# Optimization experiments

Measured on AMD Instinct MI355X. Metric: run time of the kernel, lower is better.

The kernel has to match this reference:

```python
import jax, jax.numpy as jnp
import numpy as np


def setup_inputs() -> dict:
    key = jax.random.key(0)
    kq, kk, kv, km = jax.random.split(key, 4)
    B, H, S, D = 2, 16, 2048, 64
    Q = jax.random.normal(kq, (B, H, S, D), dtype=jnp.float32)
    K = jax.random.normal(kk, (B, H, S, D), dtype=jnp.float32)
    V = jax.random.normal(kv, (B, H, S, D), dtype=jnp.float32)
    mask = jax.random.randint(km, (B, 1, S, S), 0, 2).astype(jnp.bool_)
    return {"Q": Q, "K": K, "V": V, "mask": mask}


def reference(Q, K, V, mask):
    # scores: [B, H, Sq, Sk]
    scores = jnp.einsum("bhqd,bhkd->bhqk", Q, K)
    neg = jnp.finfo(scores.dtype).min
    # Faithful to original: mask fill happens BEFORE the sqrt(d) scaling.
    scores = jnp.where(mask, neg, scores)
    inv_sqrt_d = 1.0 / jnp.sqrt(jnp.asarray(Q.shape[-1], dtype=scores.dtype))
    attn = jax.nn.softmax(scores * inv_sqrt_d, axis=-1)
    return jnp.einsum("bhqk,bhkd->bhqd", attn, V)
```

## Files before the change

kernel.cpp:

```cpp
#include <hip/hip_runtime.h>
#include <stdint.h>


#define SQ 2048
#define DH 64

using bf16x8  = __attribute__((ext_vector_type(8)))  __bf16;
using f32x4   = __attribute__((ext_vector_type(4)))  float;
using ushort8 = __attribute__((ext_vector_type(8)))  unsigned short;
using ushort4v= __attribute__((ext_vector_type(4)))  unsigned short;

static __device__ __forceinline__ unsigned short f2bf(float f) {
    union { float f; uint32_t u; } c; c.f = f;
    return (unsigned short)((c.u + 0x8000u) >> 16);
}

static __device__ __forceinline__ int swz(int row, int col) {
    return row * 64 + ((((col >> 3) ^ (row & 7))) << 3) + (col & 7);
}

static __device__ __forceinline__ f32x4 mfma16(bf16x8 a, bf16x8 b, f32x4 c) {
    return __builtin_amdgcn_mfma_f32_16x16x32_bf16(a, b, c, 0, 0, 0);
}

__global__ void pack_mask_kernel(const int* __restrict__ mask,
                                 unsigned long long* __restrict__ words, int nwords) {
    int gid = blockIdx.x * blockDim.x + threadIdx.x;
    int w = gid >> 6;
    int l = gid & 63;
    if (w < nwords) {
        int mv = mask[(size_t)w * 64 + l];
        unsigned long long b = __ballot(mv != 0);
        if (l == 0) words[w] = b;
    }
}

__global__ __launch_bounds__(256, 4)
void attn_kernel(const float* __restrict__ Q, const float* __restrict__ K,
                 const float* __restrict__ V,
                 const unsigned long long* __restrict__ Mw,
                 float* __restrict__ out) {
    __shared__ __align__(16) unsigned short Ks[64 * 64];
    __shared__ __align__(16) unsigned short Vt[64 * 64];
    __shared__ __align__(16) unsigned short Ps[4 * 16 * 64];

    const int tid  = threadIdx.x;
    const int w    = tid >> 6;
    const int l    = tid & 63;
    const int quad = l >> 4;
    const int c16  = l & 15;
    const int bx = blockIdx.x;
    const int hh = bx & 15;
    const int b  = (bx >> 4) & 1;
    const int qt = bx >> 5;

    const size_t bh = (size_t)b * 16 + hh;
    const float* Qp = Q + bh * SQ * DH;
    const float* Kp = K + bh * SQ * DH;
    const float* Vp = V + bh * SQ * DH;
    const int qw = qt * 64 + 16 * w;
    const unsigned long long* Mq = Mw + ((size_t)b * SQ + qw + quad * 4) * (SQ / 64);

    bf16x8 qf[2];
    {
        const float* qr = Qp + (size_t)(qw + c16) * DH;
        #pragma unroll
        for (int c = 0; c < 2; ++c) {
            int d0 = 32 * c + 8 * quad;
            float4 a  = *(const float4*)(qr + d0);
            float4 b4 = *(const float4*)(qr + d0 + 4);
            ushort8 t;
            t[0]=f2bf(a.x);  t[1]=f2bf(a.y);  t[2]=f2bf(a.z);  t[3]=f2bf(a.w);
            t[4]=f2bf(b4.x); t[5]=f2bf(b4.y); t[6]=f2bf(b4.z); t[7]=f2bf(b4.w);
            qf[c] = __builtin_bit_cast(bf16x8, t);
        }
    }

    f32x4 o[4];
    float lsum[4];
    #pragma unroll
    for (int i = 0; i < 4; ++i) { o[i] = (f32x4)(0.f); lsum[i] = 0.f; }

    unsigned short* Pw = Ps + w * (16 * 64);
    const int xg = (c16 & 7);

    for (int t = 0; t < 32; ++t) {
        const int kt0 = t * 64;

        unsigned long long mws[4];
        #pragma unroll
        for (int r = 0; r < 4; ++r) mws[r] = Mq[(size_t)r * (SQ / 64) + t];

        __syncthreads();

        #pragma unroll
        for (int i = 0; i < 4; ++i) {
            int idx = tid + 256 * i;
            int key = idx >> 4;
            int d0  = (idx & 15) << 2;
            float4 kv = *(const float4*)(Kp + (size_t)(kt0 + key) * DH + d0);
            ushort4v tt;
            tt[0]=f2bf(kv.x); tt[1]=f2bf(kv.y); tt[2]=f2bf(kv.z); tt[3]=f2bf(kv.w);
            *(ushort4v*)&Ks[swz(key, d0)] = tt;
        }
        #pragma unroll
        for (int p = 0; p < 4; ++p) {
            int k0l = 16 * w + 4 * p;
            const float* vb = Vp + (size_t)(kt0 + k0l) * DH + l;
            float x0 = vb[0], x1 = vb[DH], x2 = vb[2*DH], x3 = vb[3*DH];
            ushort4v tt;
            tt[0]=f2bf(x0); tt[1]=f2bf(x1); tt[2]=f2bf(x2); tt[3]=f2bf(x3);
            *(ushort4v*)&Vt[swz(l, k0l)] = tt;
        }
        __syncthreads();

        f32x4 s[4];
        #pragma unroll
        for (int i = 0; i < 4; ++i) s[i] = (f32x4)(0.f);
        #pragma unroll
        for (int c = 0; c < 2; ++c) {
            int g = ((4 * c + quad) ^ xg) << 3;
            #pragma unroll
            for (int nb = 0; nb < 4; ++nb) {
                bf16x8 kb = __builtin_bit_cast(bf16x8,
                    *(const ushort8*)&Ks[(c16 + 16 * nb) * 64 + g]);
                s[nb] = mfma16(qf[c], kb, s[nb]);
            }
        }

        #pragma unroll
        for (int r = 0; r < 4; ++r) {
            int row = quad * 4 + r;
            unsigned lo = (unsigned)mws[r];
            unsigned hi = (unsigned)(mws[r] >> 32);
            #pragma unroll
            for (int nb = 0; nb < 4; ++nb) {
                float e = __builtin_amdgcn_exp2f(fmaf(s[nb][r], 0.18033688f, -5.7707802f));
                unsigned bits = (nb & 2) ? hi : lo;
                unsigned bit  = 1u << (c16 + 16 * (nb & 1));
                float pv = (bits & bit) ? 0.0f : e;
                lsum[r] += pv;
                Pw[swz(row, c16 + 16 * nb)] = f2bf(pv);
            }
        }

        bf16x8 pa[2];
        #pragma unroll
        for (int c = 0; c < 2; ++c)
            pa[c] = __builtin_bit_cast(bf16x8,
                *(const ushort8*)&Pw[c16 * 64 + (((4 * c + quad) ^ xg) << 3)]);
        #pragma unroll
        for (int c = 0; c < 2; ++c) {
            int g = ((4 * c + quad) ^ xg) << 3;
            #pragma unroll
            for (int db = 0; db < 4; ++db) {
                bf16x8 vb = __builtin_bit_cast(bf16x8,
                    *(const ushort8*)&Vt[(c16 + 16 * db) * 64 + g]);
                o[db] = mfma16(pa[c], vb, o[db]);
            }
        }
    }

    #pragma unroll
    for (int r = 0; r < 4; ++r) {
        float v = lsum[r];
        v += __shfl_xor(v, 1, 64);
        v += __shfl_xor(v, 2, 64);
        v += __shfl_xor(v, 4, 64);
        v += __shfl_xor(v, 8, 64);
        float rinv = 1.0f / v;
        float* op = out + (bh * SQ + (size_t)(qw + quad * 4 + r)) * DH + c16;
        #pragma unroll
        for (int db = 0; db < 4; ++db) op[16 * db] = o[db][r] * rinv;
    }
}

extern "C" void kernel_launch(void* const* d_in, const int* in_sizes, int n_in,
                              void* d_out, int out_size, void* d_ws, size_t ws_size,
                              hipStream_t stream) {
    const float* Q    = (const float*)d_in[0];
    const float* K    = (const float*)d_in[1];
    const float* V    = (const float*)d_in[2];
    const int*   mask = (const int*)d_in[3];
    float* out = (float*)d_out;
    unsigned long long* mwords = (unsigned long long*)d_ws;

    const int nwords = 2 * SQ * (SQ / 64);
    pack_mask_kernel<<<dim3((nwords * 64) / 256), dim3(256), 0, stream>>>(mask, mwords, nwords);
    attn_kernel<<<dim3(1024), dim3(256), 0, stream>>>(Q, K, V, mwords, out);
}
```

Baseline: 190.6 us.

## Split key dimension across two blocks with atomic accumulation and normalize pass

```diff
diff --git a/kernel.cpp b/kernel.cpp
--- a/kernel.cpp
+++ b/kernel.cpp
@@ -39,7 +39,7 @@
 void attn_kernel(const float* __restrict__ Q, const float* __restrict__ K,
                  const float* __restrict__ V,
                  const unsigned long long* __restrict__ Mw,
-                 float* __restrict__ out) {
+                 float* __restrict__ outNum, float* __restrict__ sums) {
     __shared__ __align__(16) unsigned short Ks[64 * 64];
     __shared__ __align__(16) unsigned short Vt[64 * 64];
     __shared__ __align__(16) unsigned short Ps[4 * 16 * 64];
@@ -52,14 +52,16 @@
     const int bx = blockIdx.x;
     const int hh = bx & 15;
     const int b  = (bx >> 4) & 1;
-    const int qt = bx >> 5;
+    const int qt = (bx >> 5) & 31;
+    const int ks = bx >> 10;
 
     const size_t bh = (size_t)b * 16 + hh;
     const float* Qp = Q + bh * SQ * DH;
     const float* Kp = K + bh * SQ * DH;
     const float* Vp = V + bh * SQ * DH;
     const int qw = qt * 64 + 16 * w;
-    const unsigned long long* Mq = Mw + ((size_t)b * SQ + qw + quad * 4) * (SQ / 64);
+    const unsigned long long* Mq = Mw + ((size_t)b * SQ + qw + quad * 4) * (SQ / 64)
+                                      + ks * 16;
 
     bf16x8 qf[2];
     {
@@ -84,8 +86,8 @@
     unsigned short* Pw = Ps + w * (16 * 64);
     const int xg = (c16 & 7);
 
-    for (int t = 0; t < 32; ++t) {
-        const int kt0 = t * 64;
+    for (int t = 0; t < 16; ++t) {
+        const int kt0 = ks * 1024 + t * 64;
 
         unsigned long long mws[4];
         #pragma unroll
@@ -168,11 +170,22 @@
         v += __shfl_xor(v, 2, 64);
         v += __shfl_xor(v, 4, 64);
         v += __shfl_xor(v, 8, 64);
-        float rinv = 1.0f / v;
-        float* op = out + (bh * SQ + (size_t)(qw + quad * 4 + r)) * DH + c16;
-        #pragma unroll
-        for (int db = 0; db < 4; ++db) op[16 * db] = o[db][r] * rinv;
-    }
+        size_t rowg = bh * SQ + (size_t)(qw + quad * 4 + r);
+        float* op = outNum + rowg * DH + c16;
+        #pragma unroll
+        for (int db = 0; db < 4; ++db) atomicAdd(&op[16 * db], o[db][r]);
+        if (c16 == 0) atomicAdd(&sums[rowg], v);
+    }
+}
+
+__global__ __launch_bounds__(256)
+void normalize_kernel(float* __restrict__ out, const float* __restrict__ sums) {
+    int gid = blockIdx.x * 256 + threadIdx.x;
+    float rinv = 1.0f / sums[gid >> 4];
+    float4* o4 = (float4*)out;
+    float4 v = o4[gid];
+    v.x *= rinv; v.y *= rinv; v.z *= rinv; v.w *= rinv;
+    o4[gid] = v;
 }
 
 extern "C" void kernel_launch(void* const* d_in, const int* in_sizes, int n_in,
@@ -184,8 +197,12 @@
     const int*   mask = (const int*)d_in[3];
     float* out = (float*)d_out;
     unsigned long long* mwords = (unsigned long long*)d_ws;
+    float* sums = (float*)((char*)d_ws + (1 << 20));
 
     const int nwords = 2 * SQ * (SQ / 64);
+    hipMemsetAsync(d_out, 0, (size_t)out_size * sizeof(float), stream);
+    hipMemsetAsync(sums, 0, 32 * SQ * sizeof(float), stream);
     pack_mask_kernel<<<dim3((nwords * 64) / 256), dim3(256), 0, stream>>>(mask, mwords, nwords);
-    attn_kernel<<<dim3(1024), dim3(256), 0, stream>>>(Q, K, V, mwords, out);
-}
+    attn_kernel<<<dim3(2048), dim3(256), 0, stream>>>(Q, K, V, mwords, out, sums);
+    normalize_kernel<<<dim3(out_size / (4 * 256)), dim3(256), 0, stream>>>(out, sums);
+}
```

After: 213.0 us. +11.8%, slower.

## Pre-pack K to bf16 and V transposed, read MFMA operands from global

Applied to the files above, without the earlier changes.

```diff
diff --git a/kernel.cpp b/kernel.cpp
--- a/kernel.cpp
+++ b/kernel.cpp
@@ -35,35 +35,77 @@
     }
 }
 
-__global__ __launch_bounds__(256, 4)
-void attn_kernel(const float* __restrict__ Q, const float* __restrict__ K,
-                 const float* __restrict__ V,
+__global__ __launch_bounds__(256)
+void pack_kb_kernel(const float* __restrict__ K, unsigned short* __restrict__ Kb) {
+    size_t gid = (size_t)blockIdx.x * 256 + threadIdx.x;
+    const float* src = K + gid * 8;
+    float4 a = *(const float4*)src;
+    float4 b = *(const float4*)(src + 4);
+    ushort8 t;
+    t[0]=f2bf(a.x); t[1]=f2bf(a.y); t[2]=f2bf(a.z); t[3]=f2bf(a.w);
+    t[4]=f2bf(b.x); t[5]=f2bf(b.y); t[6]=f2bf(b.z); t[7]=f2bf(b.w);
+    *(ushort8*)(Kb + gid * 8) = t;
+}
+
+__global__ __launch_bounds__(256)
+void pack_vt_kernel(const float* __restrict__ V, unsigned short* __restrict__ Vt) {
+    __shared__ unsigned short L[64 * 68];
+    const int bx = blockIdx.x;
+    const int bh = bx >> 5;
+    const int kt = bx & 31;
+    const float* Vp = V + ((size_t)bh * SQ + kt * 64) * DH;
+    const int t = threadIdx.x;
+    #pragma unroll
+    for (int i = 0; i < 4; ++i) {
+        int idx = t + 256 * i;
+        int key = idx >> 4;
+        int d0  = (idx & 15) << 2;
+        float4 v = *(const float4*)&Vp[(size_t)key * DH + d0];
+        ushort4v u;
+        u[0]=f2bf(v.x); u[1]=f2bf(v.y); u[2]=f2bf(v.z); u[3]=f2bf(v.w);
+        *(ushort4v*)&L[key * 68 + d0] = u;
+    }
+    __syncthreads();
+    #pragma unroll
+    for (int i = 0; i < 2; ++i) {
+        int p  = t + 256 * i;
+        int d  = p >> 3;
+        int k8 = p & 7;
+        ushort8 o;
+        #pragma unroll
+        for (int j = 0; j < 8; ++j) o[j] = L[(8 * k8 + j) * 68 + d];
+        *(ushort8*)&Vt[((size_t)bh * DH + d) * SQ + kt * 64 + k8 * 8] = o;
+    }
+}
+
+__global__ __launch_bounds__(64, 2)
+void attn_kernel(const float* __restrict__ Q,
+                 const unsigned short* __restrict__ Kb,
+                 const unsigned short* __restrict__ Vt,
                  const unsigned long long* __restrict__ Mw,
                  float* __restrict__ out) {
-    __shared__ __align__(16) unsigned short Ks[64 * 64];
-    __shared__ __align__(16) unsigned short Vt[64 * 64];
-    __shared__ __align__(16) unsigned short Ps[4 * 16 * 64];
-
-    const int tid  = threadIdx.x;
-    const int w    = tid >> 6;
-    const int l    = tid & 63;
+    __shared__ __align__(16) unsigned short Ps[32 * 64];
+
+    const int l    = threadIdx.x;
     const int quad = l >> 4;
     const int c16  = l & 15;
+    const int xg   = c16 & 7;
     const int bx = blockIdx.x;
     const int hh = bx & 15;
     const int b  = (bx >> 4) & 1;
     const int qt = bx >> 5;
+    const int qw = qt * 32;
 
     const size_t bh = (size_t)b * 16 + hh;
     const float* Qp = Q + bh * SQ * DH;
-    const float* Kp = K + bh * SQ * DH;
-    const float* Vp = V + bh * SQ * DH;
-    const int qw = qt * 64 + 16 * w;
-    const unsigned long long* Mq = Mw + ((size_t)b * SQ + qw + quad * 4) * (SQ / 64);
-
-    bf16x8 qf[2];
-    {
-        const float* qr = Qp + (size_t)(qw + c16) * DH;
+    const unsigned short* Kbp = Kb + bh * SQ * DH;
+    const unsigned short* Vtp = Vt + bh * DH * SQ;
+    const unsigned long long* Mq = Mw + ((size_t)b * SQ + qw + 4 * quad) * (SQ / 64);
+
+    bf16x8 qf[2][2];
+    #pragma unroll
+    for (int f = 0; f < 2; ++f) {
+        const float* qr = Qp + (size_t)(qw + 16 * f + c16) * DH;
         #pragma unroll
         for (int c = 0; c < 2; ++c) {
             int d0 = 32 * c + 8 * quad;
@@ -72,106 +114,92 @@
             ushort8 t;
             t[0]=f2bf(a.x);  t[1]=f2bf(a.y);  t[2]=f2bf(a.z);  t[3]=f2bf(a.w);
             t[4]=f2bf(b4.x); t[5]=f2bf(b4.y); t[6]=f2bf(b4.z); t[7]=f2bf(b4.w);
-            qf[c] = __builtin_bit_cast(bf16x8, t);
-        }
-    }
-
-    f32x4 o[4];
-    float lsum[4];
-    #pragma unroll
-    for (int i = 0; i < 4; ++i) { o[i] = (f32x4)(0.f); lsum[i] = 0.f; }
-
-    unsigned short* Pw = Ps + w * (16 * 64);
-    const int xg = (c16 & 7);
+            qf[f][c] = __builtin_bit_cast(bf16x8, t);
+        }
+    }
+
+    f32x4 o[2][4];
+    float lsum[2][4];
+    #pragma unroll
+    for (int f = 0; f < 2; ++f)
+        #pragma unroll
+        for (int i = 0; i < 4; ++i) { o[f][i] = (f32x4)(0.f); lsum[f][i] = 0.f; }
 
     for (int t = 0; t < 32; ++t) {
-        const int kt0 = t * 64;
-
-        unsigned long long mws[4];
-        #pragma unroll
-        for (int r = 0; r < 4; ++r) mws[r] = Mq[(size_t)r * (SQ / 64) + t];
-
-        __syncthreads();
-
-        #pragma unroll
-        for (int i = 0; i < 4; ++i) {
-            int idx = tid + 256 * i;
-            int key = idx >> 4;
-            int d0  = (idx & 15) << 2;
-            float4 kv = *(const float4*)(Kp + (size_t)(kt0 + key) * DH + d0);
-            ushort4v tt;
-            tt[0]=f2bf(kv.x); tt[1]=f2bf(kv.y); tt[2]=f2bf(kv.z); tt[3]=f2bf(kv.w);
-            *(ushort4v*)&Ks[swz(key, d0)] = tt;
-        }
-        #pragma unroll
-        for (int p = 0; p < 4; ++p) {
-            int k0l = 16 * w + 4 * p;
-            const float* vb = Vp + (size_t)(kt0 + k0l) * DH + l;
-            float x0 = vb[0], x1 = vb[DH], x2 = vb[2*DH], x3 = vb[3*DH];
-            ushort4v tt;
-            tt[0]=f2bf(x0); tt[1]=f2bf(x1); tt[2]=f2bf(x2); tt[3]=f2bf(x3);
-            *(ushort4v*)&Vt[swz(l, k0l)] = tt;
-        }
-        __syncthreads();
-
-        f32x4 s[4];
-        #pragma unroll
-        for (int i = 0; i < 4; ++i) s[i] = (f32x4)(0.f);
+        f32x4 s[2][4];
+        #pragma unroll
+        for (int f = 0; f < 2; ++f)
+            #pragma unroll
+            for (int i = 0; i < 4; ++i) s[f][i] = (f32x4)(0.f);
+        const unsigned short* Kt = Kbp + (size_t)t * (64 * DH);
+        #pragma unroll
+        for (int c = 0; c < 2; ++c) {
+            #pragma unroll
+            for (int nb = 0; nb < 4; ++nb) {
+                bf16x8 kb = __builtin_bit_cast(bf16x8,
+                    *(const ushort8*)&Kt[(16 * nb + c16) * DH + 32 * c + 8 * quad]);
+                s[0][nb] = mfma16(qf[0][c], kb, s[0][nb]);
+                s[1][nb] = mfma16(qf[1][c], kb, s[1][nb]);
+            }
+        }
+
+        unsigned long long mws[2][4];
+        #pragma unroll
+        for (int f = 0; f < 2; ++f)
+            #pragma unroll
+            for (int r = 0; r < 4; ++r)
+                mws[f][r] = Mq[(size_t)(16 * f + r) * (SQ / 64) + t];
+
+        #pragma unroll
+        for (int f = 0; f < 2; ++f) {
+            #pragma unroll
+            for (int r = 0; r < 4; ++r) {
+                int row = 16 * f + 4 * quad + r;
+                unsigned lo = (unsigned)mws[f][r];
+                unsigned hi = (unsigned)(mws[f][r] >> 32);
+                #pragma unroll
+                for (int nb = 0; nb < 4; ++nb) {
+                    float e = __builtin_amdgcn_exp2f(
+                        fmaf(s[f][nb][r], 0.18033688f, -5.7707802f));
+                    unsigned bits = (nb & 2) ? hi : lo;
+                    unsigned bit  = 1u << (c16 + 16 * (nb & 1));
+                    float pv = (bits & bit) ? 0.0f : e;
+                    lsum[f][r] += pv;
+                    Ps[swz(row, c16 + 16 * nb)] = f2bf(pv);
+                }
+            }
+        }
+
         #pragma unroll
         for (int c = 0; c < 2; ++c) {
             int g = ((4 * c + quad) ^ xg) << 3;
-            #pragma unroll
-            for (int nb = 0; nb < 4; ++nb) {
-                bf16x8 kb = __builtin_bit_cast(bf16x8,
-                    *(const ushort8*)&Ks[(c16 + 16 * nb) * 64 + g]);
-                s[nb] = mfma16(qf[c], kb, s[nb]);
-            }
-        }
-
-        #pragma unroll
-        for (int r = 0; r < 4; ++r) {
-            int row = quad * 4 + r;
-            unsigned lo = (unsigned)mws[r];
-            unsigned hi = (unsigned)(mws[r] >> 32);
-            #pragma unroll
-            for (int nb = 0; nb < 4; ++nb) {
-                float e = __builtin_amdgcn_exp2f(fmaf(s[nb][r], 0.18033688f, -5.7707802f));
-                unsigned bits = (nb & 2) ? hi : lo;
-                unsigned bit  = 1u << (c16 + 16 * (nb & 1));
-                float pv = (bits & bit) ? 0.0f : e;
-                lsum[r] += pv;
-                Pw[swz(row, c16 + 16 * nb)] = f2bf(pv);
-            }
-        }
-
-        bf16x8 pa[2];
-        #pragma unroll
-        for (int c = 0; c < 2; ++c)
-            pa[c] = __builtin_bit_cast(bf16x8,
-                *(const ushort8*)&Pw[c16 * 64 + (((4 * c + quad) ^ xg) << 3)]);
-        #pragma unroll
-        for (int c = 0; c < 2; ++c) {
-            int g = ((4 * c + quad) ^ xg) << 3;
+            bf16x8 pa0 = __builtin_bit_cast(bf16x8, *(const ushort8*)&Ps[c16 * 64 + g]);
+            bf16x8 pa1 = __builtin_bit_cast(bf16x8, *(const ushort8*)&Ps[(16 + c16) * 64 + g]);
+            const unsigned short* Vc = Vtp + t * 64 + 32 * c + 8 * quad;
             #pragma unroll
             for (int db = 0; db < 4; ++db) {
                 bf16x8 vb = __builtin_bit_cast(bf16x8,
-                    *(const ushort8*)&Vt[(c16 + 16 * db) * 64 + g]);
-                o[db] = mfma16(pa[c], vb, o[db]);
+                    *(const ushort8*)&Vc[(size_t)(16 * db + c16) * SQ]);
+                o[0][db] = mfma16(pa0, vb, o[0][db]);
+                o[1][db] = mfma16(pa1, vb, o[1][db]);
             }
         }
     }
 
     #pragma unroll
-    for (int r = 0; r < 4; ++r) {
-        float v = lsum[r];
-        v += __shfl_xor(v, 1, 64);
-        v += __shfl_xor(v, 2, 64);
-        v += __shfl_xor(v, 4, 64);
-        v += __shfl_xor(v, 8, 64);
-        float rinv = 1.0f / v;
-        float* op = out + (bh * SQ + (size_t)(qw + quad * 4 + r)) * DH + c16;
-        #pragma unroll
-        for (int db = 0; db < 4; ++db) op[16 * db] = o[db][r] * rinv;
+    for (int f = 0; f < 2; ++f) {
+        #pragma unroll
+        for (int r = 0; r < 4; ++r) {
+            float v = lsum[f][r];
+            v += __shfl_xor(v, 1, 64);
+            v += __shfl_xor(v, 2, 64);
+            v += __shfl_xor(v, 4, 64);
+            v += __shfl_xor(v, 8, 64);
+            float rinv = 1.0f / v;
+            float* op = out + (bh * SQ + (size_t)(qw + 16 * f + 4 * quad + r)) * DH + c16;
+            #pragma unroll
+            for (int db = 0; db < 4; ++db) op[16 * db] = o[f][db][r] * rinv;
+        }
     }
 }
 
@@ -183,9 +211,15 @@
     const float* V    = (const float*)d_in[2];
     const int*   mask = (const int*)d_in[3];
     float* out = (float*)d_out;
+
     unsigned long long* mwords = (unsigned long long*)d_ws;
+    unsigned short* Kb = (unsigned short*)((char*)d_ws + (1 << 20));
+    unsigned short* Vt = (unsigned short*)((char*)d_ws + (9 << 20));
 
     const int nwords = 2 * SQ * (SQ / 64);
+    const int nelem  = 2 * 16 * SQ * DH;
     pack_mask_kernel<<<dim3((nwords * 64) / 256), dim3(256), 0, stream>>>(mask, mwords, nwords);
-    attn_kernel<<<dim3(1024), dim3(256), 0, stream>>>(Q, K, V, mwords, out);
-}
+    pack_kb_kernel<<<dim3(nelem / (8 * 256)), dim3(256), 0, stream>>>(K, Kb);
+    pack_vt_kernel<<<dim3(32 * 32), dim3(256), 0, stream>>>(V, Vt);
+    attn_kernel<<<dim3(2048), dim3(64), 0, stream>>>(Q, Kb, Vt, mwords, out);
+}
```

New measurement: 259.7 us. 36.2% more time.

## Pre-convert K/V to bf16 in prep kernel and async double-buffer K tiles

Applied to the files above, without the earlier changes.

```diff
diff --git a/kernel.cpp b/kernel.cpp
--- a/kernel.cpp
+++ b/kernel.cpp
@@ -4,6 +4,8 @@
 
 #define SQ 2048
 #define DH 64
+#define NT 32
+#define TILE_HW 4096
 
 using bf16x8  = __attribute__((ext_vector_type(8)))  __bf16;
 using f32x4   = __attribute__((ext_vector_type(4)))  float;
@@ -23,25 +25,78 @@
     return __builtin_amdgcn_mfma_f32_16x16x32_bf16(a, b, c, 0, 0, 0);
 }
 
-__global__ void pack_mask_kernel(const int* __restrict__ mask,
-                                 unsigned long long* __restrict__ words, int nwords) {
-    int gid = blockIdx.x * blockDim.x + threadIdx.x;
-    int w = gid >> 6;
-    int l = gid & 63;
-    if (w < nwords) {
-        int mv = mask[(size_t)w * 64 + l];
-        unsigned long long b = __ballot(mv != 0);
-        if (l == 0) words[w] = b;
-    }
-}
-
-__global__ __launch_bounds__(256, 4)
-void attn_kernel(const float* __restrict__ Q, const float* __restrict__ K,
+static __device__ __forceinline__ void gll16(const unsigned short* g,
+                                             unsigned short* s, int lane) {
+#if __has_builtin(__builtin_amdgcn_global_load_lds)
+    __builtin_amdgcn_global_load_lds(
+        (const __attribute__((address_space(1))) void*)g,
+        (__attribute__((address_space(3))) void*)s, 16, 0, 0);
+#else
+    *(ushort8*)(s + lane * 8) = *(const ushort8*)g;
+#endif
+}
+
+__global__ __launch_bounds__(256)
+void prep_kernel(const int* __restrict__ mask, const float* __restrict__ K,
                  const float* __restrict__ V,
+                 unsigned long long* __restrict__ words,
+                 unsigned short* __restrict__ Kb, unsigned short* __restrict__ Vt) {
+    __shared__ unsigned short L[64 * 68];
+    const int bx = blockIdx.x;
+    if (bx < 32768) {
+        int gid = bx * 256 + threadIdx.x;
+        int wd = gid >> 6, l = gid & 63;
+        int mv = mask[(size_t)wd * 64 + l];
+        unsigned long long bl = __ballot(mv != 0);
+        if (l == 0) words[wd] = bl;
+    } else if (bx < 32768 + 2048) {
+        size_t gid = (size_t)(bx - 32768) * 256 + threadIdx.x;
+        int gi = (int)(gid & 511);
+        size_t tile = gid >> 9;
+        int row = gi >> 3, j = gi & 7;
+        int col8 = ((j ^ (row & 7)) << 3);
+        const float* src = K + ((tile * 64 + row) << 6) + col8;
+        float4 a  = *(const float4*)src;
+        float4 b4 = *(const float4*)(src + 4);
+        ushort8 t;
+        t[0]=f2bf(a.x);  t[1]=f2bf(a.y);  t[2]=f2bf(a.z);  t[3]=f2bf(a.w);
+        t[4]=f2bf(b4.x); t[5]=f2bf(b4.y); t[6]=f2bf(b4.z); t[7]=f2bf(b4.w);
+        *(ushort8*)(Kb + gid * 8) = t;
+    } else {
+        int tile = bx - (32768 + 2048);
+        const float* Vp = V + (size_t)tile * 64 * 64;
+        const int t = threadIdx.x;
+        #pragma unroll
+        for (int i = 0; i < 4; ++i) {
+            int idx = t + 256 * i;
+            int key = idx >> 4;
+            int d0  = (idx & 15) << 2;
+            float4 v = *(const float4*)&Vp[(size_t)key * DH + d0];
+            ushort4v u;
+            u[0]=f2bf(v.x); u[1]=f2bf(v.y); u[2]=f2bf(v.z); u[3]=f2bf(v.w);
+            *(ushort4v*)&L[key * 68 + d0] = u;
+        }
+        __syncthreads();
+        #pragma unroll
+        for (int i = 0; i < 2; ++i) {
+            int p  = t + 256 * i;
+            int d  = p >> 3;
+            int k8 = p & 7;
+            ushort8 o;
+            #pragma unroll
+            for (int jj = 0; jj < 8; ++jj) o[jj] = L[(8 * k8 + jj) * 68 + d];
+            *(ushort8*)&Vt[((size_t)(tile >> 5) * DH + d) * SQ + (tile & 31) * 64 + k8 * 8] = o;
+        }
+    }
+}
+
+__global__ __launch_bounds__(256, 3)
+void attn_kernel(const float* __restrict__ Q,
+                 const unsigned short* __restrict__ Kb,
+                 const unsigned short* __restrict__ Vt,
                  const unsigned long long* __restrict__ Mw,
                  float* __restrict__ out) {
-    __shared__ __align__(16) unsigned short Ks[64 * 64];
-    __shared__ __align__(16) unsigned short Vt[64 * 64];
+    __shared__ __align__(16) unsigned short Ks[2][TILE_HW];
     __shared__ __align__(16) unsigned short Ps[4 * 16 * 64];
 
     const int tid  = threadIdx.x;
@@ -49,6 +104,7 @@
     const int l    = tid & 63;
     const int quad = l >> 4;
     const int c16  = l & 15;
+    const int xg   = c16 & 7;
     const int bx = blockIdx.x;
     const int hh = bx & 15;
     const int b  = (bx >> 4) & 1;
@@ -56,10 +112,10 @@
 
     const size_t bh = (size_t)b * 16 + hh;
     const float* Qp = Q + bh * SQ * DH;
-    const float* Kp = K + bh * SQ * DH;
-    const float* Vp = V + bh * SQ * DH;
+    const unsigned short* Kbp = Kb + bh * (size_t)NT * TILE_HW;
+    const unsigned short* Vtp = Vt + bh * (size_t)DH * SQ;
     const int qw = qt * 64 + 16 * w;
-    const unsigned long long* Mq = Mw + ((size_t)b * SQ + qw + quad * 4) * (SQ / 64);
+    const unsigned long long* Mq = Mw + ((size_t)b * SQ + qw + 4 * quad) * (SQ / 64);
 
     bf16x8 qf[2];
     {
@@ -82,37 +138,35 @@
     for (int i = 0; i < 4; ++i) { o[i] = (f32x4)(0.f); lsum[i] = 0.f; }
 
     unsigned short* Pw = Ps + w * (16 * 64);
-    const int xg = (c16 & 7);
-
-    for (int t = 0; t < 32; ++t) {
-        const int kt0 = t * 64;
+
+    #define STAGE_K(t_, buf_) do {                                             \
+        const unsigned short* g_ = Kbp + (size_t)(t_) * TILE_HW + (2*w)*512 + l*8; \
+        unsigned short* s_ = &Ks[buf_][2 * w * 512];                           \
+        gll16(g_, s_, l);                                                      \
+        gll16(g_ + 512, s_ + 512, l);                                          \
+    } while (0)
+
+    STAGE_K(0, 0);
+
+    for (int t = 0; t < NT; ++t) {
+        const int buf = t & 1;
+        __syncthreads();
+        if (t + 1 < NT) STAGE_K(t + 1, buf ^ 1);
 
         unsigned long long mws[4];
         #pragma unroll
         for (int r = 0; r < 4; ++r) mws[r] = Mq[(size_t)r * (SQ / 64) + t];
 
-        __syncthreads();
-
-        #pragma unroll
-        for (int i = 0; i < 4; ++i) {
-            int idx = tid + 256 * i;
-            int key = idx >> 4;
-            int d0  = (idx & 15) << 2;
-            float4 kv = *(const float4*)(Kp + (size_t)(kt0 + key) * DH + d0);
-            ushort4v tt;
-            tt[0]=f2bf(kv.x); tt[1]=f2bf(kv.y); tt[2]=f2bf(kv.z); tt[3]=f2bf(kv.w);
-            *(ushort4v*)&Ks[swz(key, d0)] = tt;
-        }
-        #pragma unroll
-        for (int p = 0; p < 4; ++p) {
-            int k0l = 16 * w + 4 * p;
-            const float* vb = Vp + (size_t)(kt0 + k0l) * DH + l;
-            float x0 = vb[0], x1 = vb[DH], x2 = vb[2*DH], x3 = vb[3*DH];
-            ushort4v tt;
-            tt[0]=f2bf(x0); tt[1]=f2bf(x1); tt[2]=f2bf(x2); tt[3]=f2bf(x3);
-            *(ushort4v*)&Vt[swz(l, k0l)] = tt;
-        }
-        __syncthreads();
+        bf16x8 vfr[2][4];
+        {
+            const unsigned short* Vc0 = Vtp + t * 64;
+            #pragma unroll
+            for (int c = 0; c < 2; ++c)
+                #pragma unroll
+                for (int db = 0; db < 4; ++db)
+                    vfr[c][db] = __builtin_bit_cast(bf16x8, *(const ushort8*)
+                        &Vc0[(size_t)(16 * db + c16) * SQ + 32 * c + 8 * quad]);
+        }
 
         f32x4 s[4];
         #pragma unroll
@@ -123,7 +177,7 @@
             #pragma unroll
             for (int nb = 0; nb < 4; ++nb) {
                 bf16x8 kb = __builtin_bit_cast(bf16x8,
-                    *(const ushort8*)&Ks[(c16 + 16 * nb) * 64 + g]);
+                    *(const ushort8*)&Ks[buf][(c16 + 16 * nb) * 64 + g]);
                 s[nb] = mfma16(qf[c], kb, s[nb]);
             }
         }
@@ -144,20 +198,13 @@
             }
         }
 
-        bf16x8 pa[2];
-        #pragma unroll
-        for (int c = 0; c < 2; ++c)
-            pa[c] = __builtin_bit_cast(bf16x8,
+        #pragma unroll
+        for (int c = 0; c < 2; ++c) {
+            bf16x8 pa = __builtin_bit_cast(bf16x8,
                 *(const ushort8*)&Pw[c16 * 64 + (((4 * c + quad) ^ xg) << 3)]);
-        #pragma unroll
-        for (int c = 0; c < 2; ++c) {
-            int g = ((4 * c + quad) ^ xg) << 3;
-            #pragma unroll
-            for (int db = 0; db < 4; ++db) {
-                bf16x8 vb = __builtin_bit_cast(bf16x8,
-                    *(const ushort8*)&Vt[(c16 + 16 * db) * 64 + g]);
-                o[db] = mfma16(pa[c], vb, o[db]);
-            }
+            #pragma unroll
+            for (int db = 0; db < 4; ++db)
+                o[db] = mfma16(pa, vfr[c][db], o[db]);
         }
     }
 
@@ -183,9 +230,12 @@
     const float* V    = (const float*)d_in[2];
     const int*   mask = (const int*)d_in[3];
     float* out = (float*)d_out;
+
     unsigned long long* mwords = (unsigned long long*)d_ws;
-
-    const int nwords = 2 * SQ * (SQ / 64);
-    pack_mask_kernel<<<dim3((nwords * 64) / 256), dim3(256), 0, stream>>>(mask, mwords, nwords);
-    attn_kernel<<<dim3(1024), dim3(256), 0, stream>>>(Q, K, V, mwords, out);
-}
+    unsigned short* Kb = (unsigned short*)((char*)d_ws + (1 << 20));
+    unsigned short* Vt = (unsigned short*)((char*)d_ws + (9 << 20));
+
+    prep_kernel<<<dim3(32768 + 2048 + 1024), dim3(256), 0, stream>>>(
+        mask, K, V, mwords, Kb, Vt);
+    attn_kernel<<<dim3(1024), dim3(256), 0, stream>>>(Q, Kb, Vt, mwords, out);
+}
```

Measured after the change: 289.3 us. +51.8%, slower.
